# Kernel optimization log

Measured on AMD Instinct MI355X. Metric: run time of the kernel, lower is better.

Reference implementation:

```python
import jax, jax.numpy as jnp
import numpy as np

B, S, D, H = 4, 4096, 2048, 512
EPS = 1e-5


def setup_inputs() -> dict:
    key = jax.random.key(0)
    ks = jax.random.split(key, 5)
    x = jax.random.normal(ks[0], (B, S, D), dtype=jnp.float32)
    ln_gamma = jnp.ones((D,), dtype=jnp.float32)
    ln_beta = jnp.zeros((D,), dtype=jnp.float32)
    # 'small' init: uniform in [1e-5 - 1e-6, 1e-5 + 1e-6]; use scaled randn here
    # so gradients are non-trivial, same math either way.
    W_down = jax.random.normal(ks[1], (H, D), dtype=jnp.float32) * 0.02
    b_down = jax.random.normal(ks[2], (H,), dtype=jnp.float32) * 0.02
    W_up = jax.random.normal(ks[3], (D, H), dtype=jnp.float32) * 0.02
    b_up = jax.random.normal(ks[4], (D,), dtype=jnp.float32) * 0.02
    return {"x": x, "ln_gamma": ln_gamma, "ln_beta": ln_beta,
            "W_down": W_down, "b_down": b_down, "W_up": W_up, "b_up": b_up}


def _layer_norm(x, gamma, beta):
    mu = jnp.mean(x, axis=-1, keepdims=True)
    var = jnp.mean(jnp.square(x - mu), axis=-1, keepdims=True)
    return (x - mu) * jax.lax.rsqrt(var + EPS) * gamma + beta


def reference(x, ln_gamma, ln_beta, W_down, b_down, W_up, b_up):
    # LayerNorm -> down-proj -> ReLU -> up-proj -> residual add
    y = _layer_norm(x, ln_gamma, ln_beta)                      # [B,S,D]
    y = jnp.einsum('bsd,hd->bsh', y, W_down) + b_down          # [B,S,H]
    y = jax.nn.relu(y)
    y = jnp.einsum('bsh,dh->bsd', y, W_up) + b_up              # [B,S,D]
    return x + y
```

## Files before the change

kernel.cpp:

```cpp
#include <hip/hip_runtime.h>

#define DD 2048
#define HH 512
#define NTOK 16384

typedef __attribute__((ext_vector_type(8))) short short8_t;
typedef __attribute__((ext_vector_type(4))) short short4_t;
typedef __attribute__((ext_vector_type(4))) float f32x4;

static __device__ __forceinline__ short f2bf(float f) {
    union { float f; unsigned u; } v; v.f = f;
    unsigned r = (v.u + 0x7fffu + ((v.u >> 16) & 1u)) >> 16;
    return (short)r;
}

static __device__ __forceinline__ void gl16(const short* g, short* l) {
    __builtin_amdgcn_global_load_lds(
        (const __attribute__((address_space(1))) unsigned int*)g,
        (__attribute__((address_space(3))) unsigned int*)l, 16, 0, 0);
}

__global__ __launch_bounds__(256) void k_wprep(
    const float* __restrict__ Wd, const float* __restrict__ g,
    const float* __restrict__ be, const float* __restrict__ Wu,
    short* __restrict__ Wg, short* __restrict__ Wub,
    float* __restrict__ c1, float* __restrict__ c2)
{
    int bid = blockIdx.x;
    if (bid < 128) {
        int w = threadIdx.x >> 6, lane = threadIdx.x & 63;
        int h = bid * 4 + w;
        const float* wr = Wd + (size_t)h * DD;
        float s1 = 0.f, s2 = 0.f;
        for (int i = 0; i < 8; i++) {
            int col = i * 256 + lane * 4;
            float4 wv = *(const float4*)(wr + col);
            float4 gv = *(const float4*)(g + col);
            float4 bv = *(const float4*)(be + col);
            s1 += gv.x * wv.x + gv.y * wv.y + gv.z * wv.z + gv.w * wv.w;
            s2 += bv.x * wv.x + bv.y * wv.y + bv.z * wv.z + bv.w * wv.w;
            short4_t o;
            o[0] = f2bf(wv.x * gv.x); o[1] = f2bf(wv.y * gv.y);
            o[2] = f2bf(wv.z * gv.z); o[3] = f2bf(wv.w * gv.w);
            *(short4_t*)(Wg + (size_t)h * DD + col) = o;
        }
        for (int m = 1; m < 64; m <<= 1) { s1 += __shfl_xor(s1, m); s2 += __shfl_xor(s2, m); }
        if (lane == 0) { c1[h] = s1; c2[h] = s2; }
    } else {
        int b = bid - 128;
        for (int r = 0; r < 4; r++) {
            int i = (b * 4 + r) * 1024 + threadIdx.x * 4;
            float4 v = *(const float4*)(Wu + i);
            short4_t o;
            o[0] = f2bf(v.x); o[1] = f2bf(v.y); o[2] = f2bf(v.z); o[3] = f2bf(v.w);
            *(short4_t*)(Wub + i) = o;
        }
    }
}

__global__ __launch_bounds__(512, 2) void k_fused(
    const float* __restrict__ x, const short* __restrict__ Wg,
    const float* __restrict__ c1, const float* __restrict__ c2,
    const float* __restrict__ bd, const short* __restrict__ Wub,
    const float* __restrict__ bu, float* __restrict__ out)
{
    __shared__ __align__(16) char smem[152064];
    short* B1   = (short*)smem;
    short* A1   = (short*)(smem + 131072);
    float* s_sum = (float*)(smem + 147456);
    float* s_sq  = (float*)(smem + 149504);
    float* s_mu  = (float*)(smem + 151552);
    float* s_rs  = (float*)(smem + 151808);
    short* Hld  = (short*)smem;
    short* B2   = (short*)(smem + 65536);

    const int tid  = threadIdx.x;
    const int lane = tid & 63;
    const int w    = tid >> 6;
    const int l15  = lane & 15;
    const int rg   = lane >> 4;
    const int m0   = blockIdx.x * 64;

    const int srow = tid >> 3;
    const int sc   = tid & 7;
    const float* xrow = x + (size_t)(m0 + srow) * DD + sc * 8;

    float psum = 0.f, psq = 0.f;
    float4 xv0, xv1;

    auto stageB1 = [&](short* buf, int kb) {
#pragma unroll
        for (int i = 0; i < 8; i++) {
            int ch = i * 512 + tid;
            int r = ch >> 3, c = ch & 7;
            gl16(Wg + (size_t)r * DD + kb + ((c ^ (r & 7)) << 3),
                 buf + (i * 512 + (w << 6)) * 8);
        }
    };
    auto loadA = [&](int kb) {
        xv0 = *(const float4*)(xrow + kb);
        xv1 = *(const float4*)(xrow + kb + 4);
    };
    auto writeA = [&](short* buf) {
        psum += xv0.x + xv0.y + xv0.z + xv0.w + xv1.x + xv1.y + xv1.z + xv1.w;
        psq  += xv0.x * xv0.x + xv0.y * xv0.y + xv0.z * xv0.z + xv0.w * xv0.w
              + xv1.x * xv1.x + xv1.y * xv1.y + xv1.z * xv1.z + xv1.w * xv1.w;
        short8_t o;
        o[0] = f2bf(xv0.x); o[1] = f2bf(xv0.y); o[2] = f2bf(xv0.z); o[3] = f2bf(xv0.w);
        o[4] = f2bf(xv1.x); o[5] = f2bf(xv1.y); o[6] = f2bf(xv1.z); o[7] = f2bf(xv1.w);
        *(short8_t*)(buf + srow * 64 + ((sc ^ (srow & 7)) << 3)) = o;
    };

    f32x4 acc[4][4];
#pragma unroll
    for (int i = 0; i < 4; i++)
#pragma unroll
        for (int j = 0; j < 4; j++) acc[i][j] = (f32x4){0.f, 0.f, 0.f, 0.f};

    stageB1(B1, 0);
    loadA(0);
    writeA(A1);
    __syncthreads();

    int cur = 0;
    for (int t = 0; t < 32; t++) {
        int nxt = cur ^ 1;
        if (t < 31) {
            stageB1(B1 + nxt * 32768, (t + 1) * 64);
            loadA((t + 1) * 64);
        }
        const short* bufA = A1 + cur * 4096;
        const short* bufB = B1 + cur * 32768;
#pragma unroll
        for (int kk = 0; kk < 2; kk++) {
            int kc = kk * 4 + rg;
            short8_t af[4], bf[4];
#pragma unroll
            for (int mi = 0; mi < 4; mi++) {
                int rr = mi * 16 + l15;
                af[mi] = *(const short8_t*)(bufA + rr * 64 + ((kc ^ (rr & 7)) << 3));
            }
#pragma unroll
            for (int ni = 0; ni < 4; ni++) {
                int rr = (w << 6) + ni * 16 + l15;
                bf[ni] = *(const short8_t*)(bufB + rr * 64 + ((kc ^ (rr & 7)) << 3));
            }
#pragma unroll
            for (int mi = 0; mi < 4; mi++)
#pragma unroll
                for (int ni = 0; ni < 4; ni++)
                    acc[mi][ni] = __builtin_amdgcn_mfma_f32_16x16x32_bf16(
                        af[mi], bf[ni], acc[mi][ni], 0, 0, 0);
        }
        if (t < 31) writeA(A1 + nxt * 4096);
        __syncthreads();
        cur = nxt;
    }

    s_sum[(srow << 3) + sc] = psum;
    s_sq[(srow << 3) + sc]  = psq;
    __syncthreads();
    if (tid < 64) {
        float s = 0.f, q = 0.f;
#pragma unroll
        for (int c = 0; c < 8; c++) { s += s_sum[(tid << 3) + c]; q += s_sq[(tid << 3) + c]; }
        float mu = s * (1.f / DD);
        float var = q * (1.f / DD) - mu * mu;
        s_mu[tid] = mu;
        s_rs[tid] = rsqrtf(var + 1e-5f);
    }
    __syncthreads();

#pragma unroll
    for (int ni = 0; ni < 4; ni++) {
        int h = (w << 6) + ni * 16 + l15;
        float C1 = c1[h];
        float C2 = c2[h] + bd[h];
#pragma unroll
        for (int mi = 0; mi < 4; mi++) {
#pragma unroll
            for (int j = 0; j < 4; j++) {
                int row = mi * 16 + rg * 4 + j;
                float v = s_rs[row] * (acc[mi][ni][j] - s_mu[row] * C1) + C2;
                v = v > 0.f ? v : 0.f;
                Hld[row * 512 + (((h >> 3) ^ (row & 7)) << 3) + (h & 7)] = f2bf(v);
            }
        }
    }

    auto stageB2 = [&](short* buf, int dp, int kb) {
#pragma unroll
        for (int i = 0; i < 4; i++) {
            int ch = i * 512 + tid;
            int r = ch >> 3, c = ch & 7;
            gl16(Wub + (size_t)(dp * 256 + r) * HH + kb + ((c ^ (r & 7)) << 3),
                 buf + (i * 512 + (w << 6)) * 8);
        }
    };

    stageB2(B2, 0, 0);
    __syncthreads();

    f32x4 acc2[4][2];
#pragma unroll
    for (int i = 0; i < 4; i++)
#pragma unroll
        for (int j = 0; j < 2; j++) acc2[i][j] = (f32x4){0.f, 0.f, 0.f, 0.f};

    cur = 0;
    for (int s = 0; s < 64; s++) {
        int nxt = cur ^ 1;
        if (s < 63) stageB2(B2 + nxt * 16384, (s + 1) >> 3, ((s + 1) & 7) * 64);
        int ks = s & 7;
        const short* bufB = B2 + cur * 16384;
#pragma unroll
        for (int kk = 0; kk < 2; kk++) {
            int kcA = (ks << 3) + kk * 4 + rg;
            int kcB = kk * 4 + rg;
            short8_t af[4], bf2[2];
#pragma unroll
            for (int mi = 0; mi < 4; mi++) {
                int rr = mi * 16 + l15;
                af[mi] = *(const short8_t*)(Hld + rr * 512 + ((kcA ^ (rr & 7)) << 3));
            }
#pragma unroll
            for (int ni = 0; ni < 2; ni++) {
                int rr = (w << 5) + ni * 16 + l15;
                bf2[ni] = *(const short8_t*)(bufB + rr * 64 + ((kcB ^ (rr & 7)) << 3));
            }
#pragma unroll
            for (int mi = 0; mi < 4; mi++)
#pragma unroll
                for (int ni = 0; ni < 2; ni++)
                    acc2[mi][ni] = __builtin_amdgcn_mfma_f32_16x16x32_bf16(
                        af[mi], bf2[ni], acc2[mi][ni], 0, 0, 0);
        }
        if (ks == 7) {
            int dp = s >> 3;
#pragma unroll
            for (int ni = 0; ni < 2; ni++) {
                int d = dp * 256 + (w << 5) + ni * 16 + l15;
                float B = bu[d];
#pragma unroll
                for (int mi = 0; mi < 4; mi++) {
#pragma unroll
                    for (int j = 0; j < 4; j++) {
                        int row = mi * 16 + rg * 4 + j;
                        size_t idx = (size_t)(m0 + row) * DD + d;
                        out[idx] = x[idx] + B + acc2[mi][ni][j];
                        acc2[mi][ni][j] = 0.f;
                    }
                }
            }
        }
        __syncthreads();
        cur = nxt;
    }
}

extern "C" void kernel_launch(void* const* d_in, const int* in_sizes, int n_in,
                              void* d_out, int out_size, void* d_ws, size_t ws_size,
                              hipStream_t stream) {
    const float* x     = (const float*)d_in[0];
    const float* gamma = (const float*)d_in[1];
    const float* beta  = (const float*)d_in[2];
    const float* Wd_f  = (const float*)d_in[3];
    const float* bd    = (const float*)d_in[4];
    const float* Wu_f  = (const float*)d_in[5];
    const float* bu    = (const float*)d_in[6];

    short* Wg  = (short*)d_ws;
    short* Wub = Wg + (size_t)HH * DD;
    float* c1  = (float*)(Wub + (size_t)DD * HH);
    float* c2  = c1 + HH;

    k_wprep<<<384, 256, 0, stream>>>(Wd_f, gamma, beta, Wu_f, Wg, Wub, c1, c2);
    k_fused<<<NTOK / 64, 512, 0, stream>>>(x, Wg, c1, c2, bd, Wub, bu, (float*)d_out);
}
```

Baseline: 142.5 us.

## Split fused LN-MLP kernel into separate down and up projection kernels

Replaces the single fused kernel, which ran 256 blocks with about 150KB of LDS each, with two kernels. The down kernel computes the LayerNorm-folded down projection over 64x256 tiles and writes a bf16 hidden tensor to workspace. The up kernel tiles the up projection as 64x512 with a smaller K step. This gives many more blocks with small LDS footprints and higher occupancy, and adds grid swizzling for cache locality. The cost is a global round trip for the hidden activations, an extra launch, and x being read twice by the down kernel (once per N-half).

```diff
diff --git a/kernel.cpp b/kernel.cpp
--- a/kernel.cpp
+++ b/kernel.cpp
@@ -58,112 +58,92 @@
     }
 }
 
-__global__ __launch_bounds__(512, 2) void k_fused(
+__global__ __launch_bounds__(512, 4) void k_down(
     const float* __restrict__ x, const short* __restrict__ Wg,
     const float* __restrict__ c1, const float* __restrict__ c2,
-    const float* __restrict__ bd, const short* __restrict__ Wub,
-    const float* __restrict__ bu, float* __restrict__ out)
+    const float* __restrict__ bd, short* __restrict__ hid)
 {
-    __shared__ __align__(16) char smem[152064];
-    short* B1   = (short*)smem;
-    short* A1   = (short*)(smem + 131072);
-    float* s_sum = (float*)(smem + 147456);
-    float* s_sq  = (float*)(smem + 149504);
-    float* s_mu  = (float*)(smem + 151552);
-    float* s_rs  = (float*)(smem + 151808);
-    short* Hld  = (short*)smem;
-    short* B2   = (short*)(smem + 65536);
-
-    const int tid  = threadIdx.x;
-    const int lane = tid & 63;
-    const int w    = tid >> 6;
-    const int l15  = lane & 15;
-    const int rg   = lane >> 4;
-    const int m0   = blockIdx.x * 64;
-
-    const int srow = tid >> 3;
-    const int sc   = tid & 7;
-    const float* xrow = x + (size_t)(m0 + srow) * DD + sc * 8;
+    __shared__ __align__(16) short sB[2][256 * 32];
+    __shared__ __align__(16) short sA[2][64 * 32];
+    __shared__ float s_ps[512], s_pq[512];
+    __shared__ float s_mu[64], s_rs[64];
+
+    int bid = blockIdx.x;
+    int nb = (bid & 7) * 64 + (bid >> 3);
+    const int m0 = (nb >> 1) * 64;
+    const int n0 = (nb & 1) * 256;
+
+    const int tid = threadIdx.x, lane = tid & 63, w = tid >> 6;
+    const int l15 = lane & 15, rg = lane >> 4;
+    const int wm = w >> 2, wn = w & 3;
+    const int arow = tid >> 3, ahalf = tid & 7;
+
+    const float* xrow = x + (size_t)(m0 + arow) * DD + ahalf * 4;
+    const int awoff = arow * 32 + (((ahalf >> 1) ^ (arow & 3)) << 3) + (ahalf & 1) * 4;
 
     float psum = 0.f, psq = 0.f;
-    float4 xv0, xv1;
-
-    auto stageB1 = [&](short* buf, int kb) {
-#pragma unroll
-        for (int i = 0; i < 8; i++) {
+    float4 xv;
+
+    auto stageB = [&](int b, int kb) {
+#pragma unroll
+        for (int i = 0; i < 2; i++) {
             int ch = i * 512 + tid;
-            int r = ch >> 3, c = ch & 7;
-            gl16(Wg + (size_t)r * DD + kb + ((c ^ (r & 7)) << 3),
-                 buf + (i * 512 + (w << 6)) * 8);
-        }
-    };
-    auto loadA = [&](int kb) {
-        xv0 = *(const float4*)(xrow + kb);
-        xv1 = *(const float4*)(xrow + kb + 4);
-    };
-    auto writeA = [&](short* buf) {
-        psum += xv0.x + xv0.y + xv0.z + xv0.w + xv1.x + xv1.y + xv1.z + xv1.w;
-        psq  += xv0.x * xv0.x + xv0.y * xv0.y + xv0.z * xv0.z + xv0.w * xv0.w
-              + xv1.x * xv1.x + xv1.y * xv1.y + xv1.z * xv1.z + xv1.w * xv1.w;
-        short8_t o;
-        o[0] = f2bf(xv0.x); o[1] = f2bf(xv0.y); o[2] = f2bf(xv0.z); o[3] = f2bf(xv0.w);
-        o[4] = f2bf(xv1.x); o[5] = f2bf(xv1.y); o[6] = f2bf(xv1.z); o[7] = f2bf(xv1.w);
-        *(short8_t*)(buf + srow * 64 + ((sc ^ (srow & 7)) << 3)) = o;
-    };
-
-    f32x4 acc[4][4];
-#pragma unroll
-    for (int i = 0; i < 4; i++)
+            int r = ch >> 2, c = ch & 3;
+            gl16(Wg + (size_t)(n0 + r) * DD + kb + ((c ^ (r & 3)) << 3),
+                 &sB[b][0] + (i * 512 + (w << 6)) * 8);
+        }
+    };
+    auto loadA = [&](int kb) { xv = *(const float4*)(xrow + kb); };
+    auto writeA = [&](int b) {
+        psum += xv.x + xv.y + xv.z + xv.w;
+        psq  += xv.x * xv.x + xv.y * xv.y + xv.z * xv.z + xv.w * xv.w;
+        short4_t o;
+        o[0] = f2bf(xv.x); o[1] = f2bf(xv.y); o[2] = f2bf(xv.z); o[3] = f2bf(xv.w);
+        *(short4_t*)(&sA[b][0] + awoff) = o;
+    };
+
+    f32x4 acc[2][4];
+#pragma unroll
+    for (int i = 0; i < 2; i++)
 #pragma unroll
         for (int j = 0; j < 4; j++) acc[i][j] = (f32x4){0.f, 0.f, 0.f, 0.f};
 
-    stageB1(B1, 0);
+    stageB(0, 0);
     loadA(0);
-    writeA(A1);
-    __syncthreads();
-
-    int cur = 0;
-    for (int t = 0; t < 32; t++) {
-        int nxt = cur ^ 1;
-        if (t < 31) {
-            stageB1(B1 + nxt * 32768, (t + 1) * 64);
-            loadA((t + 1) * 64);
-        }
-        const short* bufA = A1 + cur * 4096;
-        const short* bufB = B1 + cur * 32768;
-#pragma unroll
-        for (int kk = 0; kk < 2; kk++) {
-            int kc = kk * 4 + rg;
-            short8_t af[4], bf[4];
-#pragma unroll
-            for (int mi = 0; mi < 4; mi++) {
-                int rr = mi * 16 + l15;
-                af[mi] = *(const short8_t*)(bufA + rr * 64 + ((kc ^ (rr & 7)) << 3));
-            }
-#pragma unroll
-            for (int ni = 0; ni < 4; ni++) {
-                int rr = (w << 6) + ni * 16 + l15;
-                bf[ni] = *(const short8_t*)(bufB + rr * 64 + ((kc ^ (rr & 7)) << 3));
-            }
-#pragma unroll
-            for (int mi = 0; mi < 4; mi++)
-#pragma unroll
-                for (int ni = 0; ni < 4; ni++)
-                    acc[mi][ni] = __builtin_amdgcn_mfma_f32_16x16x32_bf16(
-                        af[mi], bf[ni], acc[mi][ni], 0, 0, 0);
-        }
-        if (t < 31) writeA(A1 + nxt * 4096);
+    writeA(0);
+    __syncthreads();
+
+    for (int t = 0; t < 64; t++) {
+        int cur = t & 1, nxt = cur ^ 1;
+        if (t < 63) { stageB(nxt, (t + 1) * 32); loadA((t + 1) * 32); }
+        short8_t af[2], bf[4];
+#pragma unroll
+        for (int mi = 0; mi < 2; mi++) {
+            int rr = wm * 32 + mi * 16 + l15;
+            af[mi] = *(const short8_t*)(&sA[cur][0] + rr * 32 + ((rg ^ (rr & 3)) << 3));
+        }
+#pragma unroll
+        for (int ni = 0; ni < 4; ni++) {
+            int rr = wn * 64 + ni * 16 + l15;
+            bf[ni] = *(const short8_t*)(&sB[cur][0] + rr * 32 + ((rg ^ (rr & 3)) << 3));
+        }
+#pragma unroll
+        for (int mi = 0; mi < 2; mi++)
+#pragma unroll
+            for (int ni = 0; ni < 4; ni++)
+                acc[mi][ni] = __builtin_amdgcn_mfma_f32_16x16x32_bf16(
+                    af[mi], bf[ni], acc[mi][ni], 0, 0, 0);
+        if (t < 63) writeA(nxt);
         __syncthreads();
-        cur = nxt;
-    }
-
-    s_sum[(srow << 3) + sc] = psum;
-    s_sq[(srow << 3) + sc]  = psq;
+    }
+
+    s_ps[tid] = psum;
+    s_pq[tid] = psq;
     __syncthreads();
     if (tid < 64) {
         float s = 0.f, q = 0.f;
 #pragma unroll
-        for (int c = 0; c < 8; c++) { s += s_sum[(tid << 3) + c]; q += s_sq[(tid << 3) + c]; }
+        for (int c = 0; c < 8; c++) { s += s_ps[tid * 8 + c]; q += s_pq[tid * 8 + c]; }
         float mu = s * (1.f / DD);
         float var = q * (1.f / DD) - mu * mu;
         s_mu[tid] = mu;
@@ -173,88 +153,101 @@
 
 #pragma unroll
     for (int ni = 0; ni < 4; ni++) {
-        int h = (w << 6) + ni * 16 + l15;
+        int h = n0 + wn * 64 + ni * 16 + l15;
         float C1 = c1[h];
         float C2 = c2[h] + bd[h];
 #pragma unroll
-        for (int mi = 0; mi < 4; mi++) {
+        for (int mi = 0; mi < 2; mi++) {
 #pragma unroll
             for (int j = 0; j < 4; j++) {
-                int row = mi * 16 + rg * 4 + j;
-                float v = s_rs[row] * (acc[mi][ni][j] - s_mu[row] * C1) + C2;
+                int rowL = wm * 32 + mi * 16 + rg * 4 + j;
+                float v = s_rs[rowL] * (acc[mi][ni][j] - s_mu[rowL] * C1) + C2;
                 v = v > 0.f ? v : 0.f;
-                Hld[row * 512 + (((h >> 3) ^ (row & 7)) << 3) + (h & 7)] = f2bf(v);
+                hid[(size_t)(m0 + rowL) * HH + h] = f2bf(v);
             }
         }
     }
-
-    auto stageB2 = [&](short* buf, int dp, int kb) {
+}
+
+__global__ __launch_bounds__(512, 4) void k_up(
+    const float* __restrict__ x, const short* __restrict__ hid,
+    const short* __restrict__ Wub, const float* __restrict__ bu,
+    float* __restrict__ out)
+{
+    __shared__ __align__(16) short sB[2][512 * 32];
+    __shared__ __align__(16) short sA[2][64 * 32];
+
+    int bid = blockIdx.x;
+    int nb = (bid & 7) * 128 + (bid >> 3);
+    const int n0 = (nb & 3) * 512;
+    const int m0 = (nb >> 2) * 64;
+
+    const int tid = threadIdx.x, lane = tid & 63, w = tid >> 6;
+    const int l15 = lane & 15, rg = lane >> 4;
+
+    auto stageB = [&](int b, int kb) {
 #pragma unroll
         for (int i = 0; i < 4; i++) {
             int ch = i * 512 + tid;
-            int r = ch >> 3, c = ch & 7;
-            gl16(Wub + (size_t)(dp * 256 + r) * HH + kb + ((c ^ (r & 7)) << 3),
-                 buf + (i * 512 + (w << 6)) * 8);
-        }
-    };
-
-    stageB2(B2, 0, 0);
-    __syncthreads();
-
-    f32x4 acc2[4][2];
+            int r = ch >> 2, c = ch & 3;
+            gl16(Wub + (size_t)(n0 + r) * HH + kb + ((c ^ (r & 3)) << 3),
+                 &sB[b][0] + (i * 512 + (w << 6)) * 8);
+        }
+    };
+    auto stageA = [&](int b, int kb) {
+        if (w < 4) {
+            int r = tid >> 2, c = tid & 3;
+            gl16(hid + (size_t)(m0 + r) * HH + kb + ((c ^ (r & 3)) << 3),
+                 &sA[b][0] + (w << 6) * 8);
+        }
+    };
+
+    f32x4 acc[4][4];
 #pragma unroll
     for (int i = 0; i < 4; i++)
 #pragma unroll
-        for (int j = 0; j < 2; j++) acc2[i][j] = (f32x4){0.f, 0.f, 0.f, 0.f};
-
-    cur = 0;
-    for (int s = 0; s < 64; s++) {
-        int nxt = cur ^ 1;
-        if (s < 63) stageB2(B2 + nxt * 16384, (s + 1) >> 3, ((s + 1) & 7) * 64);
-        int ks = s & 7;
-        const short* bufB = B2 + cur * 16384;
-#pragma unroll
-        for (int kk = 0; kk < 2; kk++) {
-            int kcA = (ks << 3) + kk * 4 + rg;
-            int kcB = kk * 4 + rg;
-            short8_t af[4], bf2[2];
-#pragma unroll
-            for (int mi = 0; mi < 4; mi++) {
-                int rr = mi * 16 + l15;
-                af[mi] = *(const short8_t*)(Hld + rr * 512 + ((kcA ^ (rr & 7)) << 3));
+        for (int j = 0; j < 4; j++) acc[i][j] = (f32x4){0.f, 0.f, 0.f, 0.f};
+
+    stageB(0, 0);
+    stageA(0, 0);
+    __syncthreads();
+
+    for (int t = 0; t < 16; t++) {
+        int cur = t & 1, nxt = cur ^ 1;
+        if (t < 15) { stageB(nxt, (t + 1) * 32); stageA(nxt, (t + 1) * 32); }
+        short8_t af[4], bf[4];
+#pragma unroll
+        for (int mi = 0; mi < 4; mi++) {
+            int rr = mi * 16 + l15;
+            af[mi] = *(const short8_t*)(&sA[cur][0] + rr * 32 + ((rg ^ (rr & 3)) << 3));
+        }
+#pragma unroll
+        for (int ni = 0; ni < 4; ni++) {
+            int rr = (w << 6) + ni * 16 + l15;
+            bf[ni] = *(const short8_t*)(&sB[cur][0] + rr * 32 + ((rg ^ (rr & 3)) << 3));
+        }
+#pragma unroll
+        for (int mi = 0; mi < 4; mi++)
+#pragma unroll
+            for (int ni = 0; ni < 4; ni++)
+                acc[mi][ni] = __builtin_amdgcn_mfma_f32_16x16x32_bf16(
+                    af[mi], bf[ni], acc[mi][ni], 0, 0, 0);
+        __syncthreads();
+    }
+
+#pragma unroll
+    for (int ni = 0; ni < 4; ni++) {
+        int d = n0 + (w << 6) + ni * 16 + l15;
+        float B = bu[d];
+#pragma unroll
+        for (int mi = 0; mi < 4; mi++) {
+#pragma unroll
+            for (int j = 0; j < 4; j++) {
+                int rowL = mi * 16 + rg * 4 + j;
+                size_t idx = (size_t)(m0 + rowL) * DD + d;
+                out[idx] = x[idx] + B + acc[mi][ni][j];
             }
-#pragma unroll
-            for (int ni = 0; ni < 2; ni++) {
-                int rr = (w << 5) + ni * 16 + l15;
-                bf2[ni] = *(const short8_t*)(bufB + rr * 64 + ((kcB ^ (rr & 7)) << 3));
-            }
-#pragma unroll
-            for (int mi = 0; mi < 4; mi++)
-#pragma unroll
-                for (int ni = 0; ni < 2; ni++)
-                    acc2[mi][ni] = __builtin_amdgcn_mfma_f32_16x16x32_bf16(
-                        af[mi], bf2[ni], acc2[mi][ni], 0, 0, 0);
-        }
-        if (ks == 7) {
-            int dp = s >> 3;
-#pragma unroll
-            for (int ni = 0; ni < 2; ni++) {
-                int d = dp * 256 + (w << 5) + ni * 16 + l15;
-                float B = bu[d];
-#pragma unroll
-                for (int mi = 0; mi < 4; mi++) {
-#pragma unroll
-                    for (int j = 0; j < 4; j++) {
-                        int row = mi * 16 + rg * 4 + j;
-                        size_t idx = (size_t)(m0 + row) * DD + d;
-                        out[idx] = x[idx] + B + acc2[mi][ni][j];
-                        acc2[mi][ni][j] = 0.f;
-                    }
-                }
-            }
-        }
-        __syncthreads();
-        cur = nxt;
+        }
     }
 }
 
@@ -273,7 +266,9 @@
     short* Wub = Wg + (size_t)HH * DD;
     float* c1  = (float*)(Wub + (size_t)DD * HH);
     float* c2  = c1 + HH;
+    short* hid = (short*)(c2 + HH);
 
     k_wprep<<<384, 256, 0, stream>>>(Wd_f, gamma, beta, Wu_f, Wg, Wub, c1, c2);
-    k_fused<<<NTOK / 64, 512, 0, stream>>>(x, Wg, c1, c2, bd, Wub, bu, (float*)d_out);
-}
+    k_down<<<(NTOK / 64) * (HH / 256), 512, 0, stream>>>(x, Wg, c1, c2, bd, hid);
+    k_up<<<(NTOK / 64) * (DD / 512), 512, 0, stream>>>(x, hid, Wub, bu, (float*)d_out);
+}
```

Result: slower. 238.8 us (+67.6%).
